# Performance work log

Hardware: AMD Instinct MI355X
Metric: run time of the kernel (lower is better)

The kernel has to match this reference:

```python
import jax, jax.numpy as jnp
import numpy as np

B, S, H = 4, 2048, 1024
NH, HD = 16, 64  # num heads, head dim


def setup_inputs() -> dict:
    key = jax.random.key(0)
    ks = jax.random.split(key, 8)
    s = 1.0 / np.sqrt(H)
    return {
        "hidden_states": jax.random.normal(ks[0], (B, S, H), jnp.float32),
        "attention_mask": jnp.zeros((B, 1, 1, S), jnp.float32),
        "Wq": jax.random.normal(ks[1], (H, H), jnp.float32) * s,
        "bq": jnp.zeros((H,), jnp.float32),
        "Wk": jax.random.normal(ks[2], (H, H), jnp.float32) * s,
        "bk": jnp.zeros((H,), jnp.float32),
        "Wv": jax.random.normal(ks[3], (H, H), jnp.float32) * s,
        "bv": jnp.zeros((H,), jnp.float32),
    }


def _split_heads(x):
    # [B, S, H] -> [B, NH, S, HD]
    return x.reshape(B, S, NH, HD).transpose(0, 2, 1, 3)


def reference(hidden_states, attention_mask, Wq, bq, Wk, bk, Wv, bv):
    q = _split_heads(hidden_states @ Wq + bq)
    k = _split_heads(hidden_states @ Wk + bk)
    v = _split_heads(hidden_states @ Wv + bv)
    scores = jnp.einsum("bhqd,bhkd->bhqk", q, k) / jnp.sqrt(jnp.float32(HD))
    probs = jax.nn.softmax(scores + attention_mask, axis=-1)  # dropout p=0 -> identity
    ctx = jnp.einsum("bhqk,bhkd->bhqd", probs, v)
    ctx = ctx.transpose(0, 2, 1, 3).reshape(B, S, H)
    return (ctx,)
```

## Files before the change

### kernel.cpp

```cpp
#include <hip/hip_runtime.h>
#include <hip/hip_bf16.h>
#include <stdint.h>


typedef unsigned short ushort_t;
typedef __attribute__((ext_vector_type(4))) float f32x4;
typedef __attribute__((ext_vector_type(8))) short short8;
typedef __attribute__((ext_vector_type(2))) unsigned int uint2v;

#define MFMA16(a, b, c) __builtin_amdgcn_mfma_f32_16x16x32_bf16((a), (b), (c), 0, 0, 0)

__device__ __forceinline__ ushort_t f2bf(float f) {
  unsigned u = __float_as_uint(f);
  u = (u + 0x7FFFu + ((u >> 16) & 1u)) >> 16;
  return (ushort_t)u;
}

typedef __attribute__((address_space(1))) unsigned int as1_uint;
typedef __attribute__((address_space(3))) unsigned int as3_uint;

__device__ __forceinline__ void async16(void* lds_dst, const void* g_src) {
  __builtin_amdgcn_global_load_lds((as1_uint*)(uintptr_t)g_src,
                                   (as3_uint*)(unsigned)(uintptr_t)lds_dst, 16, 0, 0);
}

__global__ __launch_bounds__(256) void convert_x(const float* __restrict__ X,
                                                 ushort_t* __restrict__ Xb) {
  int idx = (blockIdx.x * 256 + threadIdx.x) * 8;
  f32x4 a = *(const f32x4*)(X + idx);
  f32x4 b = *(const f32x4*)(X + idx + 4);
  short8 r;
#pragma unroll
  for (int j = 0; j < 4; ++j) r[j] = (short)f2bf(a[j]);
#pragma unroll
  for (int j = 0; j < 4; ++j) r[4 + j] = (short)f2bf(b[j]);
  *(short8*)(Xb + idx) = r;
}

__global__ __launch_bounds__(256) void convert_w(const float* __restrict__ Wq,
                                                 const float* __restrict__ Wk,
                                                 const float* __restrict__ Wv,
                                                 ushort_t* __restrict__ Wt) {
  const int mat = blockIdx.z;
  const float* W = (mat == 0) ? Wq : ((mat == 1) ? Wk : Wv);
  const int k0 = blockIdx.x * 64, n0 = blockIdx.y * 64;
  __shared__ float t[64][65];
  const int tid = threadIdx.x;
#pragma unroll
  for (int it = 0; it < 16; ++it) {
    int idx = it * 256 + tid;
    int r = idx >> 6, c = idx & 63;
    t[r][c] = W[(size_t)(k0 + r) * 1024 + n0 + c];
  }
  __syncthreads();
#pragma unroll
  for (int it = 0; it < 16; ++it) {
    int idx = it * 256 + tid;
    int nr = idx >> 6, kc = idx & 63;
    Wt[(size_t)(mat * 1024 + n0 + nr) * 1024 + k0 + kc] = f2bf(t[kc][nr]);
  }
}

__global__ __launch_bounds__(256) void gemm_qkv(const ushort_t* __restrict__ Xb,
                                                const ushort_t* __restrict__ Wt,
                                                const float* __restrict__ bq,
                                                const float* __restrict__ bk,
                                                const float* __restrict__ bv,
                                                ushort_t* __restrict__ Qb,
                                                ushort_t* __restrict__ Kb,
                                                ushort_t* __restrict__ Vt) {
  __shared__ char lds[36864];
  const int tid = threadIdx.x;
  const int l = tid & 63, w = tid >> 6;
  const int m0 = blockIdx.x * 128;
  const int n0 = blockIdx.y * 128;
  const int wm = w >> 1, wn = w & 1;

  const int lr = l >> 3;
  const int kb_log = (((l & 7) ^ lr) << 4);
  const char* srcA = (const char*)Xb + (size_t)(m0 + w * 32 + lr) * 2048 + kb_log;
  const char* srcB = (const char*)Wt + (size_t)(n0 + w * 32 + lr) * 2048 + kb_log;
  char* ldsA_w = lds + w * 4096;
  char* ldsB_w = lds + 16384 + w * 4096;

  const int ra = wm * 64 + (l & 15);
  const int rb = wn * 64 + (l & 15);
  const int swz = (l & 7) << 4;
  const int x0 = (((l >> 4) << 4)) ^ swz;
  const int x1 = (64 + ((l >> 4) << 4)) ^ swz;

  f32x4 acc[4][4];
#pragma unroll
  for (int mf = 0; mf < 4; ++mf)
#pragma unroll
    for (int nf = 0; nf < 4; ++nf) acc[mf][nf] = (f32x4){0.f, 0.f, 0.f, 0.f};

#pragma unroll 1
  for (int kt = 0; kt < 16; ++kt) {
    if (kt) __syncthreads();
    const int koff = kt * 128;
#pragma unroll
    for (int c = 0; c < 4; ++c) {
      async16(ldsA_w + c * 1024, srcA + c * 16384 + koff);
      async16(ldsB_w + c * 1024, srcB + c * 16384 + koff);
    }
    __syncthreads();
#pragma unroll
    for (int half = 0; half < 2; ++half) {
      const int xo = half ? x1 : x0;
      short8 av[4], bv2[4];
#pragma unroll
      for (int mf = 0; mf < 4; ++mf)
        av[mf] = *(const short8*)(lds + (ra + mf * 16) * 128 + xo);
#pragma unroll
      for (int nf = 0; nf < 4; ++nf)
        bv2[nf] = *(const short8*)(lds + 16384 + (rb + nf * 16) * 128 + xo);
#pragma unroll
      for (int mf = 0; mf < 4; ++mf)
#pragma unroll
        for (int nf = 0; nf < 4; ++nf)
          acc[mf][nf] = MFMA16(av[mf], bv2[nf], acc[mf][nf]);
    }
  }

  __syncthreads();
  const int col0 = n0 + wn * 64;
  const int mat = col0 >> 10;
  const int nn0 = col0 & 1023;
  const int hh = nn0 >> 6;
  const int row0 = m0 + wm * 64;
  const int bb = row0 >> 11;
  const int s0 = row0 & 2047;
  const float* bias = (mat == 0) ? bq : ((mat == 1) ? bk : bv);
  const float qscale = 0.18033688011112042f;
  if (mat < 2) {
    ushort_t* dst = (mat == 0) ? Qb : Kb;
    const float scl = (mat == 0) ? qscale : 1.0f;
#pragma unroll
    for (int mf = 0; mf < 4; ++mf)
#pragma unroll
      for (int nf = 0; nf < 4; ++nf)
#pragma unroll
        for (int i = 0; i < 4; ++i) {
          int r = mf * 16 + (l >> 4) * 4 + i;
          int d = nf * 16 + (l & 15);
          float v = (acc[mf][nf][i] + bias[nn0 + d]) * scl;
          dst[((size_t)(bb * 16 + hh) * 2048 + (s0 + r)) * 64 + d] = f2bf(v);
        }
  } else {
    ushort_t* vw = (ushort_t*)(lds + w * 9216);
#pragma unroll
    for (int mf = 0; mf < 4; ++mf)
#pragma unroll
      for (int nf = 0; nf < 4; ++nf)
#pragma unroll
        for (int i = 0; i < 4; ++i) {
          int r = mf * 16 + (l >> 4) * 4 + i;
          int d = nf * 16 + (l & 15);
          float v = acc[mf][nf][i] + bias[nn0 + d];
          vw[d * 72 + r] = f2bf(v);
        }
#pragma unroll
    for (int it = 0; it < 8; ++it) {
      int dr = it * 8 + (l >> 3);
      int sc = (l & 7) * 8;
      short8 vv = *(const short8*)((const char*)vw + dr * 144 + sc * 2);
      *(short8*)((char*)Vt + (((size_t)(bb * 16 + hh) * 64 + dr) * 2048 + s0 + sc) * 2) = vv;
    }
  }
}

__global__ __launch_bounds__(256) void attn_fwd(const ushort_t* __restrict__ Qb,
                                                const ushort_t* __restrict__ Kb,
                                                const ushort_t* __restrict__ Vt,
                                                const float* __restrict__ mask,
                                                float* __restrict__ out) {
  __shared__ char lds[49664];
  const int tid = threadIdx.x, l = tid & 63, w = tid >> 6;
  const int bh = blockIdx.y;
  const int bb = bh >> 4, hh = bh & 15;
  const int q0 = blockIdx.x * 128;
  const int lg = l >> 4, lr = l & 15;
  char* klds = lds;
  char* vlds = lds + 16384;
  char* pl = lds + 32768 + w * 4096;
  float* sbuf = (float*)(lds + 49152 + w * 128);

  const float LOG2E = 1.44269504088896340736f;
  const f32x4 fzero = (f32x4){0.f, 0.f, 0.f, 0.f};
  const int psz = (lr & 7) << 4;

  const char* qbase = (const char*)Qb + ((size_t)bh * 2048 + q0 + w * 32 + lr) * 128 + lg * 16;
  short8 aq[2][2];
  aq[0][0] = *(const short8*)(qbase);
  aq[0][1] = *(const short8*)(qbase + 64);
  aq[1][0] = *(const short8*)(qbase + 16 * 128);
  aq[1][1] = *(const short8*)(qbase + 16 * 128 + 64);

  const int srow = l >> 3;
  const int scol = ((l & 7) ^ srow) << 4;
  const char* ksrc0 = (const char*)Kb + (size_t)bh * 2048 * 128 + (size_t)(w * 16 + srow) * 128 + scol;
  const char* vsrc0 = (const char*)Vt + ((size_t)bh * 64 + w * 16 + srow) * 4096 + scol;

  {
    char* kd = klds + w * 2048;
    char* vd = vlds + w * 2048;
    async16(kd, ksrc0);
    async16(kd + 1024, ksrc0 + 1024);
    async16(vd, vsrc0);
    async16(vd + 1024, vsrc0 + 8 * 4096);
  }

  const float* mrow = mask + (size_t)bb * 2048;

  f32x4 lsum[2];
  lsum[0] = fzero;
  lsum[1] = fzero;
  f32x4 o[2][4];
#pragma unroll
  for (int qc = 0; qc < 2; ++qc)
#pragma unroll
    for (int vf = 0; vf < 4; ++vf) o[qc][vf] = fzero;

#pragma unroll 1
  for (int kt = 0; kt < 32; ++kt) {
    const int cur = kt & 1;
    asm volatile("s_waitcnt lgkmcnt(0)" ::: "memory");
    __builtin_amdgcn_s_barrier();
    if (kt < 31) {
      char* kd = klds + (cur ^ 1) * 8192 + w * 2048;
      char* vd = vlds + (cur ^ 1) * 8192 + w * 2048;
      const char* ks = ksrc0 + (size_t)(kt + 1) * 8192;
      const char* vs = vsrc0 + (kt + 1) * 128;
      async16(kd, ks);
      async16(kd + 1024, ks + 1024);
      async16(vd, vs);
      async16(vd + 1024, vs + 8 * 4096);
      asm volatile("s_waitcnt vmcnt(4)" ::: "memory");
    } else {
      asm volatile("s_waitcnt vmcnt(0)" ::: "memory");
    }
    __builtin_amdgcn_s_barrier();
    __builtin_amdgcn_sched_barrier(0);

    const char* kb = klds + cur * 8192;
    const char* vb = vlds + cur * 8192;

#pragma unroll
    for (int kf = 0; kf < 4; ++kf) {
      const char* ka = kb + (kf * 16 + lr) * 128;
      short8 a0 = *(const short8*)(ka + ((lg * 16) ^ psz));
      short8 a1 = *(const short8*)(ka + ((64 + lg * 16) ^ psz));
      f32x4 m4 = *(const f32x4*)(mrow + kt * 64 + kf * 16 + lg * 4);
#pragma unroll
      for (int qc = 0; qc < 2; ++qc) {
        f32x4 s = MFMA16(a0, aq[qc][0], fzero);
        s = MFMA16(a1, aq[qc][1], s);
        f32x4 ps;
#pragma unroll
        for (int i = 0; i < 4; ++i)
          ps[i] = __builtin_amdgcn_exp2f(fmaf(m4[i], LOG2E, s[i]));
        lsum[qc] += ps;
        unsigned w0, w1;
        asm("v_cvt_pk_bf16_f32 %0, %1, %2" : "=v"(w0) : "v"(ps[0]), "v"(ps[1]));
        asm("v_cvt_pk_bf16_f32 %0, %1, %2" : "=v"(w1) : "v"(ps[2]), "v"(ps[3]));
        uint2v pw2 = {w0, w1};
        *(uint2v*)(pl + (qc * 16 + lr) * 128 + ((kf * 32 + lg * 8) ^ psz)) = pw2;
      }
    }

    short8 pa[2][2];
#pragma unroll
    for (int qc = 0; qc < 2; ++qc) {
      pa[qc][0] = *(const short8*)(pl + (qc * 16 + lr) * 128 + ((lg * 16) ^ psz));
      pa[qc][1] = *(const short8*)(pl + (qc * 16 + lr) * 128 + ((64 + lg * 16) ^ psz));
    }
    __builtin_amdgcn_s_setprio(1);
#pragma unroll
    for (int vf = 0; vf < 4; ++vf) {
      const char* vrow = vb + (vf * 16 + lr) * 128;
      short8 v0 = *(const short8*)(vrow + ((lg * 16) ^ psz));
      short8 v1 = *(const short8*)(vrow + ((64 + lg * 16) ^ psz));
#pragma unroll
      for (int qc = 0; qc < 2; ++qc) {
        o[qc][vf] = MFMA16(pa[qc][0], v0, o[qc][vf]);
        o[qc][vf] = MFMA16(pa[qc][1], v1, o[qc][vf]);
      }
    }
    __builtin_amdgcn_s_setprio(0);
  }

#pragma unroll
  for (int qc = 0; qc < 2; ++qc) {
    float lrun = (lsum[qc][0] + lsum[qc][1]) + (lsum[qc][2] + lsum[qc][3]);
    lrun += __shfl_xor(lrun, 16);
    lrun += __shfl_xor(lrun, 32);
    if (lg == 0) sbuf[qc * 16 + lr] = lrun;
  }
#pragma unroll
  for (int qc = 0; qc < 2; ++qc) {
    f32x4 l4 = *(const f32x4*)(sbuf + qc * 16 + lg * 4);
    f32x4 inv4;
#pragma unroll
    for (int i = 0; i < 4; ++i) inv4[i] = 1.0f / l4[i];
#pragma unroll
    for (int vf = 0; vf < 4; ++vf)
#pragma unroll
      for (int i = 0; i < 4; ++i)
        out[((size_t)bb * 2048 + q0 + w * 32 + qc * 16 + lg * 4 + i) * 1024 + hh * 64 +
            vf * 16 + lr] = o[qc][vf][i] * inv4[i];
  }
}

extern "C" void kernel_launch(void* const* d_in, const int* in_sizes, int n_in,
                              void* d_out, int out_size, void* d_ws, size_t ws_size,
                              hipStream_t stream) {
  const float* hs  = (const float*)d_in[0];
  const float* msk = (const float*)d_in[1];
  const float* Wq  = (const float*)d_in[2];
  const float* bq  = (const float*)d_in[3];
  const float* Wk  = (const float*)d_in[4];
  const float* bk  = (const float*)d_in[5];
  const float* Wv  = (const float*)d_in[6];
  const float* bv  = (const float*)d_in[7];
  float* out = (float*)d_out;
  char* ws = (char*)d_ws;
  ushort_t* Xb = (ushort_t*)ws;
  ushort_t* Wt = (ushort_t*)(ws + (16u << 20));
  ushort_t* Qb = (ushort_t*)(ws + (22u << 20));
  ushort_t* Kb = (ushort_t*)(ws + (38u << 20));
  ushort_t* Vt = (ushort_t*)(ws + (54u << 20));

  convert_x<<<4096, 256, 0, stream>>>(hs, Xb);
  convert_w<<<dim3(16, 16, 3), 256, 0, stream>>>(Wq, Wk, Wv, Wt);
  gemm_qkv<<<dim3(64, 24), 256, 0, stream>>>(Xb, Wt, bq, bk, bv, Qb, Kb, Vt);
  attn_fwd<<<dim3(16, 64), 256, 0, stream>>>(Qb, Kb, Vt, msk, out);
}
```

Before: 279.0 us.

## Switch attention to 32x32 MFMA and pass P through registers instead of LDS

The attention kernel moves from 16x16x32 to 32x32x16 bf16 MFMA for both QK^T and PV. The softmax probabilities are repacked into PV operands with cross-half-wave shuffles rather than a round trip through LDS. Dropping the P scratch buffer shrinks LDS per block, and the launch bounds now request 4 blocks per CU. This aims to cut LDS traffic and instruction count and raise occupancy, at the cost of extra shuffles and more pressure on the 16-wide accumulator registers.

```diff
diff --git a/kernel.cpp b/kernel.cpp
--- a/kernel.cpp
+++ b/kernel.cpp
@@ -5,10 +5,11 @@
 
 typedef unsigned short ushort_t;
 typedef __attribute__((ext_vector_type(4))) float f32x4;
+typedef __attribute__((ext_vector_type(16))) float f32x16;
 typedef __attribute__((ext_vector_type(8))) short short8;
-typedef __attribute__((ext_vector_type(2))) unsigned int uint2v;
 
 #define MFMA16(a, b, c) __builtin_amdgcn_mfma_f32_16x16x32_bf16((a), (b), (c), 0, 0, 0)
+#define MFMA32(a, b, c) __builtin_amdgcn_mfma_f32_32x32x16_bf16((a), (b), (c), 0, 0, 0)
 
 __device__ __forceinline__ ushort_t f2bf(float f) {
   unsigned u = __float_as_uint(f);
@@ -170,32 +171,28 @@
   }
 }
 
-__global__ __launch_bounds__(256) void attn_fwd(const ushort_t* __restrict__ Qb,
-                                                const ushort_t* __restrict__ Kb,
-                                                const ushort_t* __restrict__ Vt,
-                                                const float* __restrict__ mask,
-                                                float* __restrict__ out) {
-  __shared__ char lds[49664];
+__global__ __launch_bounds__(256, 4) void attn_fwd(const ushort_t* __restrict__ Qb,
+                                                   const ushort_t* __restrict__ Kb,
+                                                   const ushort_t* __restrict__ Vt,
+                                                   const float* __restrict__ mask,
+                                                   float* __restrict__ out) {
+  __shared__ char lds[33280];
   const int tid = threadIdx.x, l = tid & 63, w = tid >> 6;
   const int bh = blockIdx.y;
   const int bb = bh >> 4, hh = bh & 15;
   const int q0 = blockIdx.x * 128;
-  const int lg = l >> 4, lr = l & 15;
+  const int l31 = l & 31, hi = l >> 5;
   char* klds = lds;
   char* vlds = lds + 16384;
-  char* pl = lds + 32768 + w * 4096;
-  float* sbuf = (float*)(lds + 49152 + w * 128);
+  float* sbuf = (float*)(lds + 32768) + w * 32;
 
   const float LOG2E = 1.44269504088896340736f;
-  const f32x4 fzero = (f32x4){0.f, 0.f, 0.f, 0.f};
-  const int psz = (lr & 7) << 4;
-
-  const char* qbase = (const char*)Qb + ((size_t)bh * 2048 + q0 + w * 32 + lr) * 128 + lg * 16;
-  short8 aq[2][2];
-  aq[0][0] = *(const short8*)(qbase);
-  aq[0][1] = *(const short8*)(qbase + 64);
-  aq[1][0] = *(const short8*)(qbase + 16 * 128);
-  aq[1][1] = *(const short8*)(qbase + 16 * 128 + 64);
+  const int psz = (l & 7) << 4;
+
+  const char* qrow = (const char*)Qb + ((size_t)bh * 2048 + q0 + w * 32 + l31) * 128 + hi * 16;
+  short8 qf[4];
+#pragma unroll
+  for (int c = 0; c < 4; ++c) qf[c] = *(const short8*)(qrow + c * 32);
 
   const int srow = l >> 3;
   const int scol = ((l & 7) ^ srow) << 4;
@@ -213,20 +210,17 @@
 
   const float* mrow = mask + (size_t)bb * 2048;
 
-  f32x4 lsum[2];
-  lsum[0] = fzero;
-  lsum[1] = fzero;
-  f32x4 o[2][4];
-#pragma unroll
-  for (int qc = 0; qc < 2; ++qc)
-#pragma unroll
-    for (int vf = 0; vf < 4; ++vf) o[qc][vf] = fzero;
+  f32x16 o0, o1;
+#pragma unroll
+  for (int i = 0; i < 16; ++i) { o0[i] = 0.f; o1[i] = 0.f; }
+  f32x4 lsum4 = (f32x4){0.f, 0.f, 0.f, 0.f};
 
 #pragma unroll 1
   for (int kt = 0; kt < 32; ++kt) {
     const int cur = kt & 1;
     asm volatile("s_waitcnt lgkmcnt(0)" ::: "memory");
     __builtin_amdgcn_s_barrier();
+    __builtin_amdgcn_sched_barrier(0);
     if (kt < 31) {
       char* kd = klds + (cur ^ 1) * 8192 + w * 2048;
       char* vd = vlds + (cur ^ 1) * 8192 + w * 2048;
@@ -243,72 +237,83 @@
     __builtin_amdgcn_s_barrier();
     __builtin_amdgcn_sched_barrier(0);
 
-    const char* kb = klds + cur * 8192;
-    const char* vb = vlds + cur * 8192;
-
-#pragma unroll
-    for (int kf = 0; kf < 4; ++kf) {
-      const char* ka = kb + (kf * 16 + lr) * 128;
-      short8 a0 = *(const short8*)(ka + ((lg * 16) ^ psz));
-      short8 a1 = *(const short8*)(ka + ((64 + lg * 16) ^ psz));
-      f32x4 m4 = *(const f32x4*)(mrow + kt * 64 + kf * 16 + lg * 4);
-#pragma unroll
-      for (int qc = 0; qc < 2; ++qc) {
-        f32x4 s = MFMA16(a0, aq[qc][0], fzero);
-        s = MFMA16(a1, aq[qc][1], s);
-        f32x4 ps;
+    const char* kbuf = klds + cur * 8192;
+    const char* vbuf = vlds + cur * 8192;
+
+#pragma unroll
+    for (int kb = 0; kb < 2; ++kb) {
+      f32x16 s;
+#pragma unroll
+      for (int i = 0; i < 16; ++i) s[i] = 0.f;
+#pragma unroll
+      for (int c = 0; c < 4; ++c) {
+        short8 kf = *(const short8*)(kbuf + (kb * 32 + l31) * 128 + ((c * 32 + hi * 16) ^ psz));
+        s = MFMA32(kf, qf[c], s);
+      }
+      f32x16 pp;
+#pragma unroll
+      for (int r2 = 0; r2 < 4; ++r2) {
+        f32x4 m4 = *(const f32x4*)(mrow + kt * 64 + kb * 32 + 8 * r2 + 4 * hi);
 #pragma unroll
         for (int i = 0; i < 4; ++i)
-          ps[i] = __builtin_amdgcn_exp2f(fmaf(m4[i], LOG2E, s[i]));
-        lsum[qc] += ps;
-        unsigned w0, w1;
-        asm("v_cvt_pk_bf16_f32 %0, %1, %2" : "=v"(w0) : "v"(ps[0]), "v"(ps[1]));
-        asm("v_cvt_pk_bf16_f32 %0, %1, %2" : "=v"(w1) : "v"(ps[2]), "v"(ps[3]));
-        uint2v pw2 = {w0, w1};
-        *(uint2v*)(pl + (qc * 16 + lr) * 128 + ((kf * 32 + lg * 8) ^ psz)) = pw2;
-      }
-    }
-
-    short8 pa[2][2];
-#pragma unroll
-    for (int qc = 0; qc < 2; ++qc) {
-      pa[qc][0] = *(const short8*)(pl + (qc * 16 + lr) * 128 + ((lg * 16) ^ psz));
-      pa[qc][1] = *(const short8*)(pl + (qc * 16 + lr) * 128 + ((64 + lg * 16) ^ psz));
-    }
-    __builtin_amdgcn_s_setprio(1);
-#pragma unroll
-    for (int vf = 0; vf < 4; ++vf) {
-      const char* vrow = vb + (vf * 16 + lr) * 128;
-      short8 v0 = *(const short8*)(vrow + ((lg * 16) ^ psz));
-      short8 v1 = *(const short8*)(vrow + ((64 + lg * 16) ^ psz));
-#pragma unroll
-      for (int qc = 0; qc < 2; ++qc) {
-        o[qc][vf] = MFMA16(pa[qc][0], v0, o[qc][vf]);
-        o[qc][vf] = MFMA16(pa[qc][1], v1, o[qc][vf]);
-      }
-    }
-    __builtin_amdgcn_s_setprio(0);
-  }
-
-#pragma unroll
-  for (int qc = 0; qc < 2; ++qc) {
-    float lrun = (lsum[qc][0] + lsum[qc][1]) + (lsum[qc][2] + lsum[qc][3]);
-    lrun += __shfl_xor(lrun, 16);
-    lrun += __shfl_xor(lrun, 32);
-    if (lg == 0) sbuf[qc * 16 + lr] = lrun;
-  }
-#pragma unroll
-  for (int qc = 0; qc < 2; ++qc) {
-    f32x4 l4 = *(const f32x4*)(sbuf + qc * 16 + lg * 4);
-    f32x4 inv4;
-#pragma unroll
-    for (int i = 0; i < 4; ++i) inv4[i] = 1.0f / l4[i];
-#pragma unroll
-    for (int vf = 0; vf < 4; ++vf)
+          pp[4 * r2 + i] = __builtin_amdgcn_exp2f(fmaf(m4[i], LOG2E, s[4 * r2 + i]));
+      }
 #pragma unroll
       for (int i = 0; i < 4; ++i)
-        out[((size_t)bb * 2048 + q0 + w * 32 + qc * 16 + lg * 4 + i) * 1024 + hh * 64 +
-            vf * 16 + lr] = o[qc][vf][i] * inv4[i];
+        lsum4[i] += ((pp[i] + pp[4 + i]) + (pp[8 + i] + pp[12 + i]));
+
+      unsigned u[8];
+#pragma unroll
+      for (int r2 = 0; r2 < 4; ++r2) {
+        asm("v_cvt_pk_bf16_f32 %0, %1, %2"
+            : "=v"(u[2 * r2]) : "v"(pp[4 * r2]), "v"(pp[4 * r2 + 1]));
+        asm("v_cvt_pk_bf16_f32 %0, %1, %2"
+            : "=v"(u[2 * r2 + 1]) : "v"(pp[4 * r2 + 2]), "v"(pp[4 * r2 + 3]));
+      }
+      short8 pa[2];
+#pragma unroll
+      for (int c = 0; c < 2; ++c) {
+        unsigned a0 = u[4 * c], b0 = u[4 * c + 2];
+        unsigned a1 = u[4 * c + 1], b1 = u[4 * c + 3];
+        unsigned s0 = hi ? a0 : b0;
+        unsigned s1 = hi ? a1 : b1;
+        unsigned r0 = (unsigned)__shfl_xor((int)s0, 32);
+        unsigned r1 = (unsigned)__shfl_xor((int)s1, 32);
+        union { unsigned uu[4]; short8 s8; } cv;
+        cv.uu[0] = hi ? r0 : a0;
+        cv.uu[1] = hi ? r1 : a1;
+        cv.uu[2] = hi ? b0 : r0;
+        cv.uu[3] = hi ? b1 : r1;
+        pa[c] = cv.s8;
+      }
+
+      __builtin_amdgcn_s_setprio(1);
+#pragma unroll
+      for (int c = 0; c < 2; ++c) {
+        const int koff = (kb * 64 + c * 32 + hi * 16) ^ psz;
+        short8 v0 = *(const short8*)(vbuf + l31 * 128 + koff);
+        short8 v1 = *(const short8*)(vbuf + (32 + l31) * 128 + koff);
+        o0 = MFMA32(pa[c], v0, o0);
+        o1 = MFMA32(pa[c], v1, o1);
+      }
+      __builtin_amdgcn_s_setprio(0);
+    }
+  }
+
+  float ls = (lsum4[0] + lsum4[1]) + (lsum4[2] + lsum4[3]);
+  float other = __shfl_xor(ls, 32);
+  float inv = 1.0f / (ls + other);
+  if (hi == 0) sbuf[l31] = inv;
+  float* obase = out + ((size_t)bb * 2048 + q0 + w * 32) * 1024 + hh * 64;
+#pragma unroll
+  for (int r2 = 0; r2 < 4; ++r2) {
+    f32x4 iv = *(const f32x4*)(sbuf + 8 * r2 + 4 * hi);
+#pragma unroll
+    for (int r0 = 0; r0 < 4; ++r0) {
+      const int q = 8 * r2 + 4 * hi + r0;
+      obase[(size_t)q * 1024 + l31] = o0[4 * r2 + r0] * iv[r0];
+      obase[(size_t)q * 1024 + 32 + l31] = o1[4 * r2 + r0] * iv[r0];
+    }
   }
 }
 
```

After: 251.8 us. -9.8%, faster.
